# Optimization experiments

Hardware: AMD Instinct MI355X
Metric: run time of the kernel (lower is better)

Reference implementation:

```python
import jax, jax.numpy as jnp
import numpy as np

FEAT, HID, HEADS, OUT, NLAYERS = 32, 64, 6, 1, 4
NG, NP, K = 16, 1000, 10
EPS_BN, EPS_IN = 1e-5, 1e-5


def _build_graph(pos, rng=None):
    # knn_graph(k=10, loop=True, batch=batch) -> to_undirected -> add_self_loops
    N = NG * NP
    parts = []
    for g in range(NG):
        off = g * NP
        p = pos[off:off + NP]
        d2 = ((p[:, None, :] - p[None, :, :]) ** 2).sum(-1)
        nbr = np.argsort(d2, axis=1)[:, :K] + off  # includes self (loop=True)
        src = nbr.reshape(-1)
        dst = np.repeat(np.arange(NP) + off, K)
        parts.append(np.stack([src, dst]))
    ei = np.concatenate(parts, axis=1)
    und = np.unique(np.concatenate([ei, ei[::-1]], axis=1).T, axis=0).T  # to_undirected (coalesced)
    loops = np.tile(np.arange(N), (2, 1))  # add_self_loops (PyG appends unconditionally)
    return np.concatenate([und, loops], axis=1).astype(np.int64)


def setup_inputs() -> dict:
    rng = np.random.default_rng(0)
    N = NG * NP
    pos = rng.standard_normal((N, 3)).astype(np.float32)
    batch = np.repeat(np.arange(NG), NP).astype(np.int64)
    edge_index = _build_graph(pos)

    def lin(fi, fo):
        return (rng.standard_normal((fi, fo)) / np.sqrt(fi)).astype(np.float32)

    HC = HEADS * HID
    z = lambda *s: jnp.zeros(s, jnp.float32)
    o = lambda *s: jnp.ones(s, jnp.float32)
    return dict(
        x=jnp.asarray(rng.standard_normal((N, FEAT)).astype(np.float32)),
        pos=jnp.asarray(pos),
        w_lin1=jnp.asarray(lin(FEAT, HID)), b_lin1=z(HID),
        w_e1=jnp.asarray(lin(1, 32)), b_e1=z(32),
        w_e2=jnp.asarray(lin(32, 1)), b_e2=z(1),
        Wl=jnp.asarray(np.stack([lin(HID, HC) for _ in range(NLAYERS)])), bl=z(NLAYERS, HC),
        Wr=jnp.asarray(np.stack([lin(HID, HC) for _ in range(NLAYERS)])), br=z(NLAYERS, HC),
        We=jnp.asarray(np.stack([lin(1, HC) for _ in range(NLAYERS)])),
        att=jnp.asarray((rng.standard_normal((NLAYERS, HEADS, HID)) / np.sqrt(HID)).astype(np.float32)),
        b_gat=z(NLAYERS, HID),
        w_emb1=jnp.asarray(lin(HID, HID)), b_emb1=z(HID),
        bn1_g=o(HID), bn1_b=z(HID), bn1_m=z(HID), bn1_v=o(HID),
        w_emb2=jnp.asarray(lin(HID, HID)), b_emb2=z(HID),
        bn2_g=o(HID), bn2_b=z(HID), bn2_m=z(HID), bn2_v=o(HID),
        w_pred=jnp.asarray(lin(HID, OUT)), b_pred=z(OUT),
        edge_index=jnp.asarray(edge_index),
        batch=jnp.asarray(batch),
        n_graphs=NG,
    )


def _bn_eval(x, g, b, m, v):
    return (x - m) / jnp.sqrt(v + EPS_BN) * g + b


def _inorm(h, batch, n_graphs):
    # PyG InstanceNorm (affine=False): per-graph, per-channel standardization
    ones = jnp.ones((h.shape[0], 1), h.dtype)
    cnt = jax.ops.segment_sum(ones, batch, num_segments=n_graphs)
    mean = jax.ops.segment_sum(h, batch, num_segments=n_graphs) / cnt
    hc = h - mean[batch]
    var = jax.ops.segment_sum(hc * hc, batch, num_segments=n_graphs) / cnt
    return hc / jnp.sqrt(var[batch] + EPS_IN)


def _gatv2(h, src, dst, ea, Wl, bl, Wr, br, We, att, bias, n):
    # GATv2Conv(heads=HEADS, concat=False, edge_dim=1)
    xl = (h @ Wl + bl).reshape(-1, HEADS, HID)  # [N,H,C] source proj
    xr = (h @ Wr + br).reshape(-1, HEADS, HID)  # [N,H,C] target proj
    e = (ea @ We).reshape(-1, HEADS, HID)       # [E,H,C] edge proj (bias=False)
    g = jax.nn.leaky_relu(xl[src] + xr[dst] + e, 0.2)
    alpha = jnp.einsum('ehc,hc->eh', g, att)    # [E,H]
    amax = jax.ops.segment_max(alpha, dst, num_segments=n)
    ex = jnp.exp(alpha - amax[dst])
    den = jax.ops.segment_sum(ex, dst, num_segments=n)
    a = ex / (den[dst] + 1e-16)                 # PyG softmax eps
    out = jax.ops.segment_sum(xl[src] * a[:, :, None], dst, num_segments=n)
    return out.mean(axis=1) + bias              # concat=False -> head mean


def reference(x, pos, w_lin1, b_lin1, w_e1, b_e1, w_e2, b_e2, Wl, bl, Wr, br, We, att, b_gat,
              w_emb1, b_emb1, bn1_g, bn1_b, bn1_m, bn1_v, w_emb2, b_emb2,
              bn2_g, bn2_b, bn2_m, bn2_v, w_pred, b_pred, edge_index, batch, n_graphs):
    src, dst = edge_index[0], edge_index[1]
    d = pos[src] - pos[dst]
    s = (d * d).sum(-1, keepdims=True)
    ew = jnp.where(s == 0, 0.0, jnp.sqrt(jnp.where(s == 0, 1.0, s)))  # safe norm (0-grad at 0)
    m = jax.nn.relu(ew @ w_e1 + b_e1)            # MLP([1,32,1]) (BN in eval = identity)
    ea = jax.nn.relu(m @ w_e2 + b_e2)            # relu(edge_MLP(.)) -> [E,1]
    h = x @ w_lin1 + b_lin1
    n = h.shape[0]
    for i in range(NLAYERS):
        h = jax.nn.relu(h + _gatv2(h, src, dst, ea, Wl[i], bl[i], Wr[i], br[i], We[i], att[i], b_gat[i], n))
        h = _inorm(h, batch, n_graphs)
    z = jax.nn.relu(h @ w_emb1 + b_emb1)
    z = _bn_eval(z, bn1_g, bn1_b, bn1_m, bn1_v)
    h_out = z @ w_emb2 + b_emb2
    pred = _bn_eval(h_out, bn2_g, bn2_b, bn2_m, bn2_v) @ w_pred + b_pred
    return h_out, pred
```

## Files before the change

### kernel.cpp

```cpp
#include <hip/hip_runtime.h>
#include <hip/hip_bf16.h>
#include <stdint.h>

typedef __hip_bfloat16 bf16;
typedef __attribute__((ext_vector_type(8))) short short8;
typedef __attribute__((ext_vector_type(4))) float float4v;
__device__ __forceinline__ float bf(const bf16 x){ return __bfloat162float(x); }
__device__ __forceinline__ float bfu(uint32_t u){ u <<= 16; return __uint_as_float(u); }
__device__ __forceinline__ unsigned short f2bs(float v){
    bf16 b = __float2bfloat16(v);
    return *(unsigned short*)&b;
}

#define FEAT    32
#define HID     64
#define HEADS   6
#define HC      384
#define NLAYERS 4
#define NG      16
#define NP      1000
#define NN      16000
#define EPS_BN  1e-5f
#define EPS_IN  1e-5f
#define LOG2E   1.44269504f
#define STATSZ  (2*NG*HID)
#define NBLK    (NN/4)
#define NTILES  48
#define WPKSZ   (NLAYERS*NTILES*64*16)
#define XSTR    772

__device__ __forceinline__ float normv(float v, const float* st, int g, int c){
    if (!st) return v;
    float s  = st[g*HID + c];
    float s2 = st[NG*HID + g*HID + c];
    float mean = s*(1.f/NP);
    float var  = fmaxf(s2*(1.f/NP) - mean*mean, 0.f);
    return (v - mean)*rsqrtf(var + EPS_IN);
}

__global__ void sentinel_kernel(float* out, int n, float val){
    int i = blockIdx.x*256 + threadIdx.x;
    if (i < n) out[i] = val;
}

__global__ void zero_detect_kernel(int* meta, int n, const int* ei){
    if ((int)blockIdx.x == (int)gridDim.x - 1){
        __shared__ int nz;
        if (threadIdx.x == 0) nz = 0;
        __syncthreads();
        for (int i = 1 + 2*threadIdx.x; i < 1024; i += 512)
            if (ei[i] != 0) atomicAdd(&nz, 1);
        __syncthreads();
        if (threadIdx.x == 0) meta[0] = (nz == 0) ? 1 : 0;
    } else {
        int i = blockIdx.x*256 + threadIdx.x;
        if (i < n) meta[64 + i] = 0;
    }
}

__device__ __forceinline__ int load_idx(const int* ei, int idx, int mode){
    if (mode) return (int)((const long long*)ei)[idx];
    return ei[idx];
}

__global__ void count_kernel(const int* ei, const int* mode, int* deg, int E){
    int e = blockIdx.x*256 + threadIdx.x;
    if (e >= E) return;
    int d = load_idx(ei, E + e, *mode);
    if (d >= 0 && d < NN) atomicAdd(&deg[d], 1);
}

__global__ void scan_kernel(const int* deg, int* rowptr, int N){
    __shared__ int part[256];
    __shared__ int offs[256];
    int t = threadIdx.x;
    int chunk = (N + 255)/256;
    int lo = t*chunk, hi = lo + chunk; if (hi > N) hi = N;
    int s = 0;
    for (int i = lo; i < hi; i++) s += deg[i];
    part[t] = s;
    __syncthreads();
    if (t == 0){
        int r = 0;
        for (int i = 0; i < 256; i++){ offs[i] = r; r += part[i]; }
        rowptr[N] = r;
    }
    __syncthreads();
    int r = offs[t];
    for (int i = lo; i < hi; i++){ rowptr[i] = r; r += deg[i]; }
}

__global__ void scatter_ea_kernel(const int* ei, const float* pos,
                                  const float* w_e1, const float* b_e1,
                                  const float* w_e2, const float* b_e2,
                                  const int* rowptr, int* fill, const int* mode_p,
                                  int* csr_src, float* ea_csr, int E){
    int e = blockIdx.x*256 + threadIdx.x;
    if (e >= E) return;
    int mode = *mode_p;
    int s = load_idx(ei, e, mode);
    int d = load_idx(ei, E + e, mode);
    if (s < 0 || s >= NN || d < 0 || d >= NN) return;
    float dx = pos[s*3+0] - pos[d*3+0];
    float dy = pos[s*3+1] - pos[d*3+1];
    float dz = pos[s*3+2] - pos[d*3+2];
    float ss = dx*dx + dy*dy + dz*dz;
    float ew = (ss == 0.f) ? 0.f : sqrtf(ss);
    float acc = b_e2[0];
    #pragma unroll
    for (int j = 0; j < 32; j++){
        float m = ew*w_e1[j] + b_e1[j];
        m = m > 0.f ? m : 0.f;
        acc += m*w_e2[j];
    }
    acc = acc > 0.f ? acc : 0.f;
    int p = rowptr[d] + atomicAdd(&fill[d], 1);
    if (p < 0 || p >= E) return;
    csr_src[p] = s;
    ea_csr[p] = acc;
}

__global__ void lin1_wpack_kernel(const float* __restrict__ x,
                                  const float* __restrict__ w1,
                                  const float* __restrict__ b1,
                                  float* __restrict__ h, int N, int nb_lin,
                                  const float* __restrict__ Wl,
                                  const float* __restrict__ Wr,
                                  short* __restrict__ wpk){
    if ((int)blockIdx.x < nb_lin){
        int tid = blockIdx.x*256 + threadIdx.x;
        if (tid >= N*HID) return;
        int n = tid >> 6, c = tid & 63;
        float acc = b1[c];
        #pragma unroll
        for (int k = 0; k < FEAT; k++) acc += x[n*FEAT+k] * w1[k*HID+c];
        h[tid] = acc;
    } else {
        int idx = (blockIdx.x - nb_lin)*256 + threadIdx.x;
        if (idx >= NLAYERS*NTILES*64) return;
        int layer = idx / (NTILES*64);
        int r = idx - layer*NTILES*64;
        int t = r >> 6, lane = r & 63;
        int q = lane >> 4, m = lane & 15;
        int col = t*16 + m;
        bool isR = col >= HC;
        int c2 = isR ? col - HC : col;
        const float* W = (isR ? Wr : Wl) + (size_t)layer*HID*HC;
        unsigned short out[16];
        #pragma unroll
        for (int s = 0; s < 2; s++)
            #pragma unroll
            for (int j = 0; j < 8; j++)
                out[s*8+j] = f2bs(W[(size_t)(s*32 + q*8 + j)*HC + c2]);
        short8* dst = (short8*)(wpk + (size_t)idx*16);
        dst[0] = *(short8*)&out[0];
        dst[1] = *(short8*)&out[8];
    }
}

__global__ __launch_bounds__(256) void xlxr_mfma_kernel(
        const float* __restrict__ h, const float* __restrict__ statPrev,
        const short* __restrict__ wpk,
        const float* __restrict__ bl, const float* __restrict__ br,
        bf16* __restrict__ xl, bf16* __restrict__ xr, int layer){
    __shared__ unsigned short lds[16*XSTR];
    int n0 = blockIdx.x*16;
    int wave = threadIdx.x >> 6;
    int lane = threadIdx.x & 63;
    int q = lane >> 4;
    int m = lane & 15;
    int node = n0 + m;
    int g = node / NP;

    short8 afrag[2];
    #pragma unroll
    for (int s = 0; s < 2; s++){
        const float4* hp4 = (const float4*)(h + (size_t)node*HID + s*32 + q*8);
        float4 va = hp4[0], vb = hp4[1];
        int cb = s*32 + q*8;
        afrag[s][0] = (short)f2bs(normv(va.x, statPrev, g, cb+0));
        afrag[s][1] = (short)f2bs(normv(va.y, statPrev, g, cb+1));
        afrag[s][2] = (short)f2bs(normv(va.z, statPrev, g, cb+2));
        afrag[s][3] = (short)f2bs(normv(va.w, statPrev, g, cb+3));
        afrag[s][4] = (short)f2bs(normv(vb.x, statPrev, g, cb+4));
        afrag[s][5] = (short)f2bs(normv(vb.y, statPrev, g, cb+5));
        afrag[s][6] = (short)f2bs(normv(vb.z, statPrev, g, cb+6));
        afrag[s][7] = (short)f2bs(normv(vb.w, statPrev, g, cb+7));
    }

    const float* blp = bl + (size_t)layer*HC;
    const float* brp = br + (size_t)layer*HC;

    for (int t = wave*12; t < wave*12 + 12; t++){
        const short8* bsrc = (const short8*)(wpk + ((size_t)(layer*NTILES + t)*64 + lane)*16);
        short8 b0 = bsrc[0], b1 = bsrc[1];
        float4v acc = {0.f, 0.f, 0.f, 0.f};
        acc = __builtin_amdgcn_mfma_f32_16x16x32_bf16(afrag[0], b0, acc, 0, 0, 0);
        acc = __builtin_amdgcn_mfma_f32_16x16x32_bf16(afrag[1], b1, acc, 0, 0, 0);
        int col = t*16 + m;
        bool isR = col >= HC;
        int c2 = isR ? col - HC : col;
        float bias = isR ? brp[c2] : blp[c2];
        #pragma unroll
        for (int r = 0; r < 4; r++)
            lds[(q*4 + r)*XSTR + col] = f2bs(acc[r] + bias);
    }
    __syncthreads();
    for (int i = threadIdx.x; i < 16*48; i += 256){
        int row = i / 48, seg = i - row*48;
        unsigned short tmp[8];
        #pragma unroll
        for (int j = 0; j < 8; j++) tmp[j] = lds[row*XSTR + seg*8 + j];
        *(uint4*)(xl + (size_t)(n0+row)*HC + seg*8) = *(uint4*)tmp;
    }
    for (int i = threadIdx.x; i < 16*48; i += 256){
        int row = i / 48, seg = i - row*48;
        unsigned short tmp[8];
        #pragma unroll
        for (int j = 0; j < 8; j++) tmp[j] = lds[row*XSTR + 384 + seg*8 + j];
        *(uint4*)(xr + (size_t)(n0+row)*HC + seg*8) = *(uint4*)tmp;
    }
}

__global__ __launch_bounds__(256) void agg_kernel(
        const bf16* __restrict__ xl, const bf16* __restrict__ xr,
        const int* __restrict__ rowptr,
        const int* __restrict__ csr_src,
        const float* __restrict__ ea_csr,
        const float* __restrict__ We, const float* __restrict__ att,
        const float* __restrict__ b_gat,
        float* __restrict__ h,
        const float* __restrict__ statPrev, float* __restrict__ partial,
        int layer){
    int wave = threadIdx.x >> 6, lane = threadIdx.x & 63;
    int n = blockIdx.x*4 + wave;
    int g = n / NP;
    int r0 = rowptr[n];
    int deg = rowptr[n+1] - r0;

    __shared__ float ps[4][2][HID];

    int grp = lane >> 3, li = lane & 7;
    bool active = grp < HEADS;
    int cb = active ? (grp*HID + li*8) : 0;

    float xrr[8], wer[8], atr[8];
    if (active){
        const uint4* xru = (const uint4*)(xr + (size_t)n*HC);
        uint4 u = xru[grp*8 + li];
        xrr[0]=bfu(u.x&0xffffu); xrr[1]=bfu(u.x>>16);
        xrr[2]=bfu(u.y&0xffffu); xrr[3]=bfu(u.y>>16);
        xrr[4]=bfu(u.z&0xffffu); xrr[5]=bfu(u.z>>16);
        xrr[6]=bfu(u.w&0xffffu); xrr[7]=bfu(u.w>>16);
    }
    #pragma unroll
    for (int i = 0; i < 8; i++){
        wer[i] = We[layer*HC + cb + i];
        atr[i] = att[layer*HC + cb + i]*LOG2E;
    }

    float m_ = -1e30f, l_ = 0.f;
    float acc[8];
    #pragma unroll
    for (int i = 0; i < 8; i++) acc[i] = 0.f;

    const uint4* xlu = (const uint4*)xl;
    int voff = grp*8 + li;

    if (active){
        int j = 0;
        for (; j + 1 < deg; j += 2){
            int sa = csr_src[r0 + j], sb = csr_src[r0 + j + 1];
            float eva = ea_csr[r0 + j], evb = ea_csr[r0 + j + 1];
            uint4 ua = xlu[(size_t)sa*48 + voff];
            uint4 ub = xlu[(size_t)sb*48 + voff];
            float xa[8], xb[8];
            xa[0]=bfu(ua.x&0xffffu); xa[1]=bfu(ua.x>>16);
            xa[2]=bfu(ua.y&0xffffu); xa[3]=bfu(ua.y>>16);
            xa[4]=bfu(ua.z&0xffffu); xa[5]=bfu(ua.z>>16);
            xa[6]=bfu(ua.w&0xffffu); xa[7]=bfu(ua.w>>16);
            xb[0]=bfu(ub.x&0xffffu); xb[1]=bfu(ub.x>>16);
            xb[2]=bfu(ub.y&0xffffu); xb[3]=bfu(ub.y>>16);
            xb[4]=bfu(ub.z&0xffffu); xb[5]=bfu(ub.z>>16);
            xb[6]=bfu(ub.w&0xffffu); xb[7]=bfu(ub.w>>16);
            float ca = 0.f, cb_ = 0.f;
            #pragma unroll
            for (int i = 0; i < 8; i++){
                float ga = xa[i] + xrr[i] + eva*wer[i];
                ga = fmaxf(ga, 0.2f*ga);
                ca += ga*atr[i];
                float gb = xb[i] + xrr[i] + evb*wer[i];
                gb = fmaxf(gb, 0.2f*gb);
                cb_ += gb*atr[i];
            }
            #pragma unroll
            for (int mm = 1; mm <= 4; mm <<= 1){
                ca  += __shfl_xor(ca, mm);
                cb_ += __shfl_xor(cb_, mm);
            }
            float mn = fmaxf(fmaxf(m_, ca), cb_);
            float r  = exp2f(m_ - mn);
            float pa = exp2f(ca - mn);
            float pb = exp2f(cb_ - mn);
            l_ = l_*r + pa + pb;
            #pragma unroll
            for (int i = 0; i < 8; i++) acc[i] = acc[i]*r + pa*xa[i] + pb*xb[i];
            m_ = mn;
        }
        if (j < deg){
            int sa = csr_src[r0 + j];
            float eva = ea_csr[r0 + j];
            uint4 ua = xlu[(size_t)sa*48 + voff];
            float xa[8];
            xa[0]=bfu(ua.x&0xffffu); xa[1]=bfu(ua.x>>16);
            xa[2]=bfu(ua.y&0xffffu); xa[3]=bfu(ua.y>>16);
            xa[4]=bfu(ua.z&0xffffu); xa[5]=bfu(ua.z>>16);
            xa[6]=bfu(ua.w&0xffffu); xa[7]=bfu(ua.w>>16);
            float ca = 0.f;
            #pragma unroll
            for (int i = 0; i < 8; i++){
                float ga = xa[i] + xrr[i] + eva*wer[i];
                ga = fmaxf(ga, 0.2f*ga);
                ca += ga*atr[i];
            }
            #pragma unroll
            for (int mm = 1; mm <= 4; mm <<= 1) ca += __shfl_xor(ca, mm);
            float mn = fmaxf(m_, ca);
            float r  = exp2f(m_ - mn);
            float pa = exp2f(ca - mn);
            l_ = l_*r + pa;
            #pragma unroll
            for (int i = 0; i < 8; i++) acc[i] = acc[i]*r + pa*xa[i];
            m_ = mn;
        }
    }

    float v[8];
    float rl = active ? 1.f/(l_ + 1e-16f) : 0.f;
    #pragma unroll
    for (int i = 0; i < 8; i++) v[i] = acc[i]*rl;
    #pragma unroll
    for (int mm = 8; mm <= 32; mm <<= 1)
        #pragma unroll
        for (int i = 0; i < 8; i++) v[i] += __shfl_xor(v[i], mm);

    if (lane < 8){
        int c0 = lane*8;
        const float4* hp4 = (const float4*)(h + (size_t)n*HID + c0);
        float4 h0 = hp4[0], h1 = hp4[1];
        float hv[8] = {h0.x,h0.y,h0.z,h0.w,h1.x,h1.y,h1.z,h1.w};
        float o[8];
        #pragma unroll
        for (int i = 0; i < 8; i++){
            float r = normv(hv[i], statPrev, g, c0+i)
                    + v[i]*(1.f/HEADS) + b_gat[layer*HID + c0 + i];
            o[i] = r > 0.f ? r : 0.f;
            ps[wave][0][c0+i] = o[i];
            ps[wave][1][c0+i] = o[i]*o[i];
        }
        float4* out4 = (float4*)(h + (size_t)n*HID + c0);
        out4[0] = make_float4(o[0],o[1],o[2],o[3]);
        out4[1] = make_float4(o[4],o[5],o[6],o[7]);
    }
    __syncthreads();
    if (threadIdx.x < HID){
        int c = threadIdx.x;
        float s  = ps[0][0][c] + ps[1][0][c] + ps[2][0][c] + ps[3][0][c];
        float s2 = ps[0][1][c] + ps[1][1][c] + ps[2][1][c] + ps[3][1][c];
        partial[(size_t)blockIdx.x*128 + c]      = s;
        partial[(size_t)blockIdx.x*128 + 64 + c] = s2;
    }
}

__global__ void stat_reduce_kernel(const float* __restrict__ partial,
                                   float* __restrict__ stat){
    int idx = blockIdx.x*256 + threadIdx.x;
    if (idx >= NG*HID*4) return;
    int slice = idx & 3;
    int gc = idx >> 2;
    int g = gc >> 6, c = gc & 63;
    int b0 = g*(NP/4);
    float s = 0.f, s2 = 0.f;
    for (int b = slice; b < NP/4; b += 4){
        s  += partial[(size_t)(b0+b)*128 + c];
        s2 += partial[(size_t)(b0+b)*128 + 64 + c];
    }
    s  += __shfl_xor(s, 1);  s  += __shfl_xor(s, 2);
    s2 += __shfl_xor(s2, 1); s2 += __shfl_xor(s2, 2);
    if (slice == 0){
        stat[g*HID + c] = s;
        stat[NG*HID + g*HID + c] = s2;
    }
}

__global__ __launch_bounds__(256) void final_kernel(
        const float* __restrict__ h, const float* __restrict__ statPrev,
        const float* w1, const float* b1,
        const float* g1, const float* be1, const float* m1, const float* v1,
        const float* w2, const float* b2,
        const float* g2, const float* be2, const float* m2, const float* v2,
        const float* wp, const float* bp,
        float* out, int N){
    int wave = threadIdx.x >> 6, c = threadIdx.x & 63;
    int n = blockIdx.x*4 + wave;
    __shared__ float hr[4][HID], zr[4][HID];
    hr[wave][c] = normv(h[(size_t)n*HID + c], statPrev, n/NP, c);
    __syncthreads();
    float z = b1[c];
    #pragma unroll 8
    for (int k = 0; k < HID; k++) z += hr[wave][k]*w1[k*HID+c];
    z = z > 0.f ? z : 0.f;
    z = (z - m1[c]) / sqrtf(v1[c] + EPS_BN) * g1[c] + be1[c];
    zr[wave][c] = z;
    __syncthreads();
    float ho = b2[c];
    #pragma unroll 8
    for (int k = 0; k < HID; k++) ho += zr[wave][k]*w2[k*HID+c];
    out[(size_t)n*HID + c] = ho;
    float t = (ho - m2[c]) / sqrtf(v2[c] + EPS_BN) * g2[c] + be2[c];
    float p = t * wp[c];
    #pragma unroll
    for (int m = 32; m >= 1; m >>= 1) p += __shfl_xor(p, m);
    if (c == 0) out[(size_t)N*HID + n] = p + bp[0];
}

extern "C" void kernel_launch(void* const* d_in, const int* in_sizes, int n_in,
                              void* d_out, int out_size, void* d_ws, size_t ws_size,
                              hipStream_t stream){
    const float* x      = (const float*)d_in[0];
    const float* pos    = (const float*)d_in[1];
    const float* w_lin1 = (const float*)d_in[2];
    const float* b_lin1 = (const float*)d_in[3];
    const float* w_e1   = (const float*)d_in[4];
    const float* b_e1   = (const float*)d_in[5];
    const float* w_e2   = (const float*)d_in[6];
    const float* b_e2   = (const float*)d_in[7];
    const float* Wl     = (const float*)d_in[8];
    const float* bl     = (const float*)d_in[9];
    const float* Wr     = (const float*)d_in[10];
    const float* br     = (const float*)d_in[11];
    const float* We     = (const float*)d_in[12];
    const float* att    = (const float*)d_in[13];
    const float* b_gat  = (const float*)d_in[14];
    const float* w_emb1 = (const float*)d_in[15];
    const float* b_emb1 = (const float*)d_in[16];
    const float* bn1_g  = (const float*)d_in[17];
    const float* bn1_b  = (const float*)d_in[18];
    const float* bn1_m  = (const float*)d_in[19];
    const float* bn1_v  = (const float*)d_in[20];
    const float* w_emb2 = (const float*)d_in[21];
    const float* b_emb2 = (const float*)d_in[22];
    const float* bn2_g  = (const float*)d_in[23];
    const float* bn2_b  = (const float*)d_in[24];
    const float* bn2_m  = (const float*)d_in[25];
    const float* bn2_v  = (const float*)d_in[26];
    const float* w_pred = (const float*)d_in[27];
    const float* b_pred = (const float*)d_in[28];
    const int*   ei     = (const int*)d_in[29];

    const int N = in_sizes[0] / FEAT;
    const int E = in_sizes[29] / 2;
    int ob = (out_size + 255)/256;

    bool ok = (n_in >= 32) && (N == NN) && (E > N)
           && (in_sizes[1]  == 3*N)
           && (in_sizes[8]  == NLAYERS*HID*HC)
           && (in_sizes[13] == NLAYERS*HEADS*HID)
           && (in_sizes[27] == HID)
           && (out_size == N*HID + N);
    if (!ok){
        sentinel_kernel<<<ob, 256, 0, stream>>>((float*)d_out, out_size, 4000.0f);
        return;
    }

    char* p = (char*)d_ws;
    auto carve = [&](size_t bytes)->void*{
        void* r = (void*)p;
        p += (bytes + 255) & ~(size_t)255;
        return r;
    };
    int*   meta   = (int*)  carve((size_t)(2*N + 64)*4);
    float* stats  = (float*)carve((size_t)NLAYERS*STATSZ*4);
    float* partial= (float*)carve((size_t)NBLK*128*4);
    short* wpk    = (short*)carve((size_t)WPKSZ*2);
    int*   rowptr = (int*)  carve((size_t)(N+1)*4);
    int*   csr_src= (int*)  carve((size_t)E*4);
    float* ea_csr = (float*)carve((size_t)E*4);
    float* h      = (float*)carve((size_t)N*HID*4);
    bf16*  xl     = (bf16*) carve((size_t)N*HC*2);
    bf16*  xr     = (bf16*) carve((size_t)N*HC*2);
    size_t used = (size_t)(p - (char*)d_ws);

    if (used > ws_size){
        sentinel_kernel<<<ob, 256, 0, stream>>>((float*)d_out, out_size,
                                                5000.0f + (float)(ws_size >> 20));
        return;
    }

    int* mode = meta;
    int* deg  = meta + 64;
    int* fill = meta + 64 + N;

    int zb = (2*N + 255)/256 + 1;
    zero_detect_kernel<<<zb, 256, 0, stream>>>(meta, 2*N, ei);

    int eb = (E + 255)/256;
    count_kernel<<<eb, 256, 0, stream>>>(ei, mode, deg, E);
    scan_kernel<<<1, 256, 0, stream>>>(deg, rowptr, N);
    scatter_ea_kernel<<<eb, 256, 0, stream>>>(ei, pos, w_e1, b_e1, w_e2, b_e2,
                                              rowptr, fill, mode, csr_src, ea_csr, E);

    int nb = (N*HID + 255)/256;
    int wb = (NLAYERS*NTILES*64 + 255)/256;
    lin1_wpack_kernel<<<nb + wb, 256, 0, stream>>>(x, w_lin1, b_lin1, h, N, nb,
                                                   Wl, Wr, wpk);

    for (int l = 0; l < NLAYERS; l++){
        const float* statPrev = (l == 0) ? nullptr : stats + (size_t)(l-1)*STATSZ;
        float* statCur = stats + (size_t)l*STATSZ;
        xlxr_mfma_kernel<<<N/16, 256, 0, stream>>>(h, statPrev, wpk, bl, br,
                                                   xl, xr, l);
        agg_kernel<<<N/4, 256, 0, stream>>>(xl, xr, rowptr, csr_src, ea_csr,
                                            We, att, b_gat, h,
                                            statPrev, partial, l);
        stat_reduce_kernel<<<(NG*HID*4 + 255)/256, 256, 0, stream>>>(partial, statCur);
    }

    final_kernel<<<N/4, 256, 0, stream>>>(h, stats + (size_t)(NLAYERS-1)*STATSZ,
        w_emb1, b_emb1, bn1_g, bn1_b, bn1_m, bn1_v,
        w_emb2, b_emb2, bn2_g, bn2_b, bn2_m, bn2_v,
        w_pred, b_pred, (float*)d_out, N);
}
```

Measured before the change: 531.9 us.

## Drop LDS staging in xlxr kernel and shuffle-broadcast edge indices in aggregation

```diff
diff --git a/kernel.cpp b/kernel.cpp
--- a/kernel.cpp
+++ b/kernel.cpp
@@ -27,7 +27,6 @@
 #define NBLK    (NN/4)
 #define NTILES  48
 #define WPKSZ   (NLAYERS*NTILES*64*16)
-#define XSTR    772
 
 __device__ __forceinline__ float normv(float v, const float* st, int g, int c){
     if (!st) return v;
@@ -163,7 +162,6 @@
         const short* __restrict__ wpk,
         const float* __restrict__ bl, const float* __restrict__ br,
         bf16* __restrict__ xl, bf16* __restrict__ xr, int layer){
-    __shared__ unsigned short lds[16*XSTR];
     int n0 = blockIdx.x*16;
     int wave = threadIdx.x >> 6;
     int lane = threadIdx.x & 63;
@@ -201,24 +199,12 @@
         bool isR = col >= HC;
         int c2 = isR ? col - HC : col;
         float bias = isR ? brp[c2] : blp[c2];
+        bf16* dst = isR ? xr : xl;
         #pragma unroll
-        for (int r = 0; r < 4; r++)
-            lds[(q*4 + r)*XSTR + col] = f2bs(acc[r] + bias);
-    }
-    __syncthreads();
-    for (int i = threadIdx.x; i < 16*48; i += 256){
-        int row = i / 48, seg = i - row*48;
-        unsigned short tmp[8];
-        #pragma unroll
-        for (int j = 0; j < 8; j++) tmp[j] = lds[row*XSTR + seg*8 + j];
-        *(uint4*)(xl + (size_t)(n0+row)*HC + seg*8) = *(uint4*)tmp;
-    }
-    for (int i = threadIdx.x; i < 16*48; i += 256){
-        int row = i / 48, seg = i - row*48;
-        unsigned short tmp[8];
-        #pragma unroll
-        for (int j = 0; j < 8; j++) tmp[j] = lds[row*XSTR + 384 + seg*8 + j];
-        *(uint4*)(xr + (size_t)(n0+row)*HC + seg*8) = *(uint4*)tmp;
+        for (int r = 0; r < 4; r++){
+            int row = q*4 + r;
+            dst[(size_t)(n0 + row)*HC + c2] = __float2bfloat16(acc[r] + bias);
+        }
     }
 }
 
@@ -267,71 +253,76 @@
     const uint4* xlu = (const uint4*)xl;
     int voff = grp*8 + li;
 
-    if (active){
-        int j = 0;
-        for (; j + 1 < deg; j += 2){
-            int sa = csr_src[r0 + j], sb = csr_src[r0 + j + 1];
-            float eva = ea_csr[r0 + j], evb = ea_csr[r0 + j + 1];
-            uint4 ua = xlu[(size_t)sa*48 + voff];
-            uint4 ub = xlu[(size_t)sb*48 + voff];
-            float xa[8], xb[8];
-            xa[0]=bfu(ua.x&0xffffu); xa[1]=bfu(ua.x>>16);
-            xa[2]=bfu(ua.y&0xffffu); xa[3]=bfu(ua.y>>16);
-            xa[4]=bfu(ua.z&0xffffu); xa[5]=bfu(ua.z>>16);
-            xa[6]=bfu(ua.w&0xffffu); xa[7]=bfu(ua.w>>16);
-            xb[0]=bfu(ub.x&0xffffu); xb[1]=bfu(ub.x>>16);
-            xb[2]=bfu(ub.y&0xffffu); xb[3]=bfu(ub.y>>16);
-            xb[4]=bfu(ub.z&0xffffu); xb[5]=bfu(ub.z>>16);
-            xb[6]=bfu(ub.w&0xffffu); xb[7]=bfu(ub.w>>16);
-            float ca = 0.f, cb_ = 0.f;
-            #pragma unroll
-            for (int i = 0; i < 8; i++){
-                float ga = xa[i] + xrr[i] + eva*wer[i];
-                ga = fmaxf(ga, 0.2f*ga);
-                ca += ga*atr[i];
-                float gb = xb[i] + xrr[i] + evb*wer[i];
-                gb = fmaxf(gb, 0.2f*gb);
-                cb_ += gb*atr[i];
+    for (int t0 = 0; t0 < deg; t0 += 64){
+        int nch = min(64, deg - t0);
+        int   sreg = (lane < nch) ? csr_src[r0 + t0 + lane] : 0;
+        float ereg = (lane < nch) ? ea_csr[r0 + t0 + lane] : 0.f;
+        if (active){
+            int j = 0;
+            for (; j + 1 < nch; j += 2){
+                int sa = __shfl(sreg, j), sb = __shfl(sreg, j + 1);
+                float eva = __shfl(ereg, j), evb = __shfl(ereg, j + 1);
+                uint4 ua = xlu[(size_t)sa*48 + voff];
+                uint4 ub = xlu[(size_t)sb*48 + voff];
+                float xa[8], xb[8];
+                xa[0]=bfu(ua.x&0xffffu); xa[1]=bfu(ua.x>>16);
+                xa[2]=bfu(ua.y&0xffffu); xa[3]=bfu(ua.y>>16);
+                xa[4]=bfu(ua.z&0xffffu); xa[5]=bfu(ua.z>>16);
+                xa[6]=bfu(ua.w&0xffffu); xa[7]=bfu(ua.w>>16);
+                xb[0]=bfu(ub.x&0xffffu); xb[1]=bfu(ub.x>>16);
+                xb[2]=bfu(ub.y&0xffffu); xb[3]=bfu(ub.y>>16);
+                xb[4]=bfu(ub.z&0xffffu); xb[5]=bfu(ub.z>>16);
+                xb[6]=bfu(ub.w&0xffffu); xb[7]=bfu(ub.w>>16);
+                float ca = 0.f, cb_ = 0.f;
+                #pragma unroll
+                for (int i = 0; i < 8; i++){
+                    float ga = xa[i] + xrr[i] + eva*wer[i];
+                    ga = fmaxf(ga, 0.2f*ga);
+                    ca += ga*atr[i];
+                    float gb = xb[i] + xrr[i] + evb*wer[i];
+                    gb = fmaxf(gb, 0.2f*gb);
+                    cb_ += gb*atr[i];
+                }
+                #pragma unroll
+                for (int mm = 1; mm <= 4; mm <<= 1){
+                    ca  += __shfl_xor(ca, mm);
+                    cb_ += __shfl_xor(cb_, mm);
+                }
+                float mn = fmaxf(fmaxf(m_, ca), cb_);
+                float r  = exp2f(m_ - mn);
+                float pa = exp2f(ca - mn);
+                float pb = exp2f(cb_ - mn);
+                l_ = l_*r + pa + pb;
+                #pragma unroll
+                for (int i = 0; i < 8; i++) acc[i] = acc[i]*r + pa*xa[i] + pb*xb[i];
+                m_ = mn;
             }
-            #pragma unroll
-            for (int mm = 1; mm <= 4; mm <<= 1){
-                ca  += __shfl_xor(ca, mm);
-                cb_ += __shfl_xor(cb_, mm);
+            if (j < nch){
+                int sa = __shfl(sreg, j);
+                float eva = __shfl(ereg, j);
+                uint4 ua = xlu[(size_t)sa*48 + voff];
+                float xa[8];
+                xa[0]=bfu(ua.x&0xffffu); xa[1]=bfu(ua.x>>16);
+                xa[2]=bfu(ua.y&0xffffu); xa[3]=bfu(ua.y>>16);
+                xa[4]=bfu(ua.z&0xffffu); xa[5]=bfu(ua.z>>16);
+                xa[6]=bfu(ua.w&0xffffu); xa[7]=bfu(ua.w>>16);
+                float ca = 0.f;
+                #pragma unroll
+                for (int i = 0; i < 8; i++){
+                    float ga = xa[i] + xrr[i] + eva*wer[i];
+                    ga = fmaxf(ga, 0.2f*ga);
+                    ca += ga*atr[i];
+                }
+                #pragma unroll
+                for (int mm = 1; mm <= 4; mm <<= 1) ca += __shfl_xor(ca, mm);
+                float mn = fmaxf(m_, ca);
+                float r  = exp2f(m_ - mn);
+                float pa = exp2f(ca - mn);
+                l_ = l_*r + pa;
+                #pragma unroll
+                for (int i = 0; i < 8; i++) acc[i] = acc[i]*r + pa*xa[i];
+                m_ = mn;
             }
-            float mn = fmaxf(fmaxf(m_, ca), cb_);
-            float r  = exp2f(m_ - mn);
-            float pa = exp2f(ca - mn);
-            float pb = exp2f(cb_ - mn);
-            l_ = l_*r + pa + pb;
-            #pragma unroll
-            for (int i = 0; i < 8; i++) acc[i] = acc[i]*r + pa*xa[i] + pb*xb[i];
-            m_ = mn;
-        }
-        if (j < deg){
-            int sa = csr_src[r0 + j];
-            float eva = ea_csr[r0 + j];
-            uint4 ua = xlu[(size_t)sa*48 + voff];
-            float xa[8];
-            xa[0]=bfu(ua.x&0xffffu); xa[1]=bfu(ua.x>>16);
-            xa[2]=bfu(ua.y&0xffffu); xa[3]=bfu(ua.y>>16);
-            xa[4]=bfu(ua.z&0xffffu); xa[5]=bfu(ua.z>>16);
-            xa[6]=bfu(ua.w&0xffffu); xa[7]=bfu(ua.w>>16);
-            float ca = 0.f;
-            #pragma unroll
-            for (int i = 0; i < 8; i++){
-                float ga = xa[i] + xrr[i] + eva*wer[i];
-                ga = fmaxf(ga, 0.2f*ga);
-                ca += ga*atr[i];
-            }
-            #pragma unroll
-            for (int mm = 1; mm <= 4; mm <<= 1) ca += __shfl_xor(ca, mm);
-            float mn = fmaxf(m_, ca);
-            float r  = exp2f(m_ - mn);
-            float pa = exp2f(ca - mn);
-            l_ = l_*r + pa;
-            #pragma unroll
-            for (int i = 0; i < 8; i++) acc[i] = acc[i]*r + pa*xa[i];
-            m_ = mn;
         }
     }
 
```

Result: faster. 503.2 us (-5.4%).
